# Optimization experiments

Hardware: AMD Instinct MI355X
Metric: run time of the kernel (lower is better)

Reference implementation:

```python
import jax, jax.numpy as jnp
import numpy as np
import math

N_HEAD = 32
HEAD_DIM = 64
ROTARY_DIM = 32
ROTARY_BASE = 10000.0
NEG_INF = -10000.0


def _rope_cos_sin(seqlen):
    # RotaryEmbedding._update_cos_sin_cache: inv_freq over even indices of rotary_dim
    inv_freq = 1.0 / (ROTARY_BASE ** (jnp.arange(0, ROTARY_DIM, 2, dtype=jnp.float32) / ROTARY_DIM))
    t = jnp.arange(seqlen, dtype=jnp.float32)
    freqs = jnp.outer(t, inv_freq)  # [s, rd/2]
    return jnp.cos(freqs), jnp.sin(freqs)


def _apply_rotary(t, cos, sin):
    # t: [b, s, h, d]; GPT-NeoX half-rotation on first ROTARY_DIM dims, pass-through rest
    half = ROTARY_DIM // 2
    x1 = t[..., :half]
    x2 = t[..., half:ROTARY_DIM]
    x_pass = t[..., ROTARY_DIM:]
    c = cos[:, None, :]  # [s, 1, rd/2] -> broadcasts over (b, s, h, rd/2)
    s_ = sin[:, None, :]
    return jnp.concatenate([x1 * c - x2 * s_, x1 * s_ + x2 * c, x_pass], axis=-1)


def setup_inputs() -> dict:
    key = jax.random.key(0)
    k1, k2, k3, k4, k5 = jax.random.split(key, 5)
    b, s, e = 2, 2048, 2048
    return {
        "x": jax.random.normal(k1, (b, s, e), dtype=jnp.float32),
        "Wqkv": jax.random.normal(k2, (e, 3 * e), dtype=jnp.float32) * 0.02,
        "bqkv": jax.random.normal(k3, (3 * e,), dtype=jnp.float32) * 0.02,
        "Wout": jax.random.normal(k4, (e, e), dtype=jnp.float32) * 0.02,
        "bout": jax.random.normal(k5, (e,), dtype=jnp.float32) * 0.02,
    }


def reference(x, Wqkv, bqkv, Wout, bout):
    b, s, e = x.shape
    # QKV projection -> [b, s, 3, h, d]
    qkv = (x @ Wqkv + bqkv).reshape(b, s, 3, N_HEAD, HEAD_DIM)
    cos, sin = _rope_cos_sin(s)
    q = _apply_rotary(qkv[:, :, 0], cos, sin)
    k = _apply_rotary(qkv[:, :, 1], cos, sin)
    v = qkv[:, :, 2]
    # Attention (SelfAttention/CrossAttention math, fp32, materialized scores)
    scale = 1.0 / math.sqrt(HEAD_DIM)
    scores = jnp.einsum('bthd,bshd->bhts', q, k * scale)  # [b, h, s, s]
    rows = jnp.arange(s)[:, None]
    cols = jnp.arange(s)[None, :]
    causal_mask = cols > rows  # seqlen_q == seqlen_k
    scores = jnp.where(causal_mask, NEG_INF, scores)
    attn = jax.nn.softmax(scores, axis=-1)
    out = jnp.einsum('bhts,bshd->bthd', attn, v).reshape(b, s, e)
    return out @ Wout + bout
```

## Files before the change

### kernel.cpp

```cpp
#include <hip/hip_runtime.h>


typedef _Float16 half8 __attribute__((ext_vector_type(8)));
typedef _Float16 half4 __attribute__((ext_vector_type(4)));
typedef float floatx4 __attribute__((ext_vector_type(4)));

#define GLD_LDS16(gp, sp)                                        \
  __builtin_amdgcn_global_load_lds(                              \
      (__attribute__((address_space(1))) void*)(gp),             \
      (__attribute__((address_space(3))) void*)(sp), 16, 0, 0)

__device__ __forceinline__ floatx4 mfma16(half8 a, half8 b, floatx4 c) {
  return __builtin_amdgcn_mfma_f32_16x16x32_f16(a, b, c, 0, 0, 0);
}
__device__ __forceinline__ floatx4 mfma16k16(half4 a, half4 b, floatx4 c) {
  return __builtin_amdgcn_mfma_f32_16x16x16f16(a, b, c, 0, 0, 0);
}

__global__ __launch_bounds__(256) void cvt_x_kernel(const float* __restrict__ x,
                                                    _Float16* __restrict__ xh) {
  int idx = blockIdx.x * 256 + threadIdx.x;
  const floatx4* p = (const floatx4*)x + (size_t)idx * 2;
  floatx4 a = p[0], b = p[1];
  half8 o;
#pragma unroll
  for (int j = 0; j < 4; ++j) { o[j] = (_Float16)a[j]; o[4 + j] = (_Float16)b[j]; }
  *((half8*)xh + idx) = o;
}

__global__ __launch_bounds__(256) void cvt_wt_kernel(const float* __restrict__ W,
                                                     _Float16* __restrict__ Wt,
                                                     int Kd, int Nd) {
  __shared__ float tile[64][65];
  int n0 = blockIdx.x * 64, k0 = blockIdx.y * 64;
  int tid = threadIdx.x;
#pragma unroll
  for (int it = 0; it < 4; ++it) {
    int r = (tid >> 4) + it * 16;
    int c = (tid & 15) * 4;
    floatx4 v = *(const floatx4*)(W + (size_t)(k0 + r) * Nd + n0 + c);
    tile[r][c + 0] = v[0]; tile[r][c + 1] = v[1];
    tile[r][c + 2] = v[2]; tile[r][c + 3] = v[3];
  }
  __syncthreads();
#pragma unroll
  for (int it = 0; it < 2; ++it) {
    int r = (tid >> 3) + it * 32;
    int c = (tid & 7) * 8;
    half8 o;
#pragma unroll
    for (int j = 0; j < 8; ++j) o[j] = (_Float16)tile[c + j][r];
    *(half8*)(Wt + (size_t)(n0 + r) * Kd + k0 + c) = o;
  }
}

template <int MODE>
__global__ __launch_bounds__(256) void gemm_f16_kernel(
    const _Float16* __restrict__ A, const _Float16* __restrict__ Bt,
    const float* __restrict__ bias, int Kd, int Nd,
    _Float16* __restrict__ Qd, _Float16* __restrict__ Kkd,
    _Float16* __restrict__ Vd, float* __restrict__ Co) {
  __shared__ __align__(16) _Float16 sA[128 * 64];
  __shared__ __align__(16) _Float16 sB[128 * 64];
  int tid = threadIdx.x, w = tid >> 6, l = tid & 63;
  int lr = l & 15, lq = l >> 4;
  int m0 = blockIdx.y * 128, n0 = blockIdx.x * 128;
  int wrow = (w >> 1) * 64, wcol = (w & 1) * 64;

  floatx4 z4 = {0.f, 0.f, 0.f, 0.f};
  floatx4 acc[4][4];
#pragma unroll
  for (int i = 0; i < 4; ++i)
#pragma unroll
    for (int j = 0; j < 4; ++j) acc[i][j] = z4;

  int srow = l >> 3;
  int slot = (l & 7) ^ srow;
  const _Float16* aG = A + (size_t)(m0 + w * 32 + srow) * Kd + slot * 8;
  const _Float16* bG = Bt + (size_t)(n0 + w * 32 + srow) * Kd + slot * 8;
  _Float16* sAw = &sA[w * 2048];
  _Float16* sBw = &sB[w * 2048];

  for (int kt = 0; kt < Kd; kt += 64) {
#pragma unroll
    for (int t = 0; t < 4; ++t) {
      GLD_LDS16(aG + (size_t)t * 8 * Kd + kt, sAw + t * 512);
      GLD_LDS16(bG + (size_t)t * 8 * Kd + kt, sBw + t * 512);
    }
    __syncthreads();
#pragma unroll
    for (int ks = 0; ks < 2; ++ks) {
      half8 af[4], bf[4];
#pragma unroll
      for (int i = 0; i < 4; ++i) {
        int ar = wrow + i * 16 + lr;
        int br = wcol + i * 16 + lr;
        int sl = (((ks << 2) | lq) ^ (lr & 7)) * 8;
        af[i] = *(const half8*)&sA[ar * 64 + sl];
        bf[i] = *(const half8*)&sB[br * 64 + sl];
      }
#pragma unroll
      for (int i = 0; i < 4; ++i)
#pragma unroll
        for (int j = 0; j < 4; ++j) acc[i][j] = mfma16(af[i], bf[j], acc[i][j]);
    }
    __syncthreads();
  }

  if (MODE == 0) {
    int which = n0 >> 11;
    _Float16* dst = (which == 0) ? Qd : (which == 1) ? Kkd : Vd;
#pragma unroll
    for (int j = 0; j < 4; ++j) {
      int n = n0 + wcol + j * 16 + lr;
      float bj = bias[n];
      int hh = (n & 2047) >> 6, dd = n & 63;
#pragma unroll
      for (int i = 0; i < 4; ++i)
#pragma unroll
        for (int r = 0; r < 4; ++r) {
          int m = m0 + wrow + i * 16 + lq * 4 + r;
          int bb = m >> 11, t = m & 2047;
          dst[((size_t)(bb * 32 + hh) * 2048 + (size_t)t) * 64 + dd] =
              (_Float16)(acc[i][j][r] + bj);
        }
    }
  } else {
#pragma unroll
    for (int j = 0; j < 4; ++j) {
      int n = n0 + wcol + j * 16 + lr;
      float bj = bias[n];
#pragma unroll
      for (int i = 0; i < 4; ++i)
#pragma unroll
        for (int r = 0; r < 4; ++r) {
          int m = m0 + wrow + i * 16 + lq * 4 + r;
          Co[(size_t)m * Nd + n] = acc[i][j][r] + bj;
        }
    }
  }
}

__global__ __launch_bounds__(256) void rope_kernel(_Float16* __restrict__ Qp,
                                                   _Float16* __restrict__ Kp) {
  int idx = blockIdx.x * 256 + threadIdx.x;
  int t = idx & 2047;
  int bh = (idx >> 11) & 63;
  _Float16* base = ((idx >> 17) ? Kp : Qp) + ((size_t)bh * 2048 + t) * 64;
  half8* hp = (half8*)base;
  half8 h0 = hp[0], h1 = hp[1], h2 = hp[2], h3 = hp[3];
  float v[32];
#pragma unroll
  for (int j = 0; j < 8; ++j) {
    v[j] = (float)h0[j];      v[8 + j] = (float)h1[j];
    v[16 + j] = (float)h2[j]; v[24 + j] = (float)h3[j];
  }
  float o[32];
#pragma unroll
  for (int j = 0; j < 16; ++j) {
    float freq = __expf(-(float)j * 0.57564627324851148f);
    float ang = (float)t * freq;
    float cs = cosf(ang), sn = sinf(ang);
    o[j] = v[j] * cs - v[j + 16] * sn;
    o[j + 16] = v[j] * sn + v[j + 16] * cs;
  }
  half8 g0, g1, g2, g3;
#pragma unroll
  for (int j = 0; j < 8; ++j) {
    g0[j] = (_Float16)o[j];      g1[j] = (_Float16)o[8 + j];
    g2[j] = (_Float16)o[16 + j]; g3[j] = (_Float16)o[24 + j];
  }
  hp[0] = g0; hp[1] = g1; hp[2] = g2; hp[3] = g3;
}

__global__ __launch_bounds__(256) void vtrans_kernel(const _Float16* __restrict__ V,
                                                     _Float16* __restrict__ Vt) {
  __shared__ __align__(16) _Float16 tile[64][72];
  int s0 = blockIdx.x * 64;
  int bh = blockIdx.y;
  const _Float16* Vb = V + (size_t)bh * 2048 * 64;
  _Float16* Vtb = Vt + (size_t)bh * 64 * 2048;
  int tid = threadIdx.x;
#pragma unroll
  for (int it = 0; it < 2; ++it) {
    int r = (tid >> 3) + it * 32;
    int cc = (tid & 7) * 8;
    *(half8*)&tile[r][cc] = *(const half8*)(Vb + (size_t)(s0 + r) * 64 + cc);
  }
  __syncthreads();
#pragma unroll
  for (int it = 0; it < 2; ++it) {
    int r = (tid >> 3) + it * 32;
    int cc = (tid & 7) * 8;
    half8 o;
#pragma unroll
    for (int j = 0; j < 8; ++j) o[j] = tile[cc + j][r];
    *(half8*)(Vtb + (size_t)r * 2048 + s0 + cc) = o;
  }
}

__global__ __launch_bounds__(256, 3) void attn_kernel(
    const _Float16* __restrict__ Q, const _Float16* __restrict__ Kk,
    const _Float16* __restrict__ Vt, _Float16* __restrict__ O) {
  constexpr int S = 2048;
  int bh = blockIdx.x;
  int qt = 15 - (int)blockIdx.y;
  int bb = bh >> 5, hh = bh & 31;
  const _Float16* Qb = Q + (size_t)bh * S * 64;
  const _Float16* Kb = Kk + (size_t)bh * S * 64;
  const _Float16* Vb = Vt + (size_t)bh * 64 * S;

  __shared__ __align__(16) _Float16 sK[128 * 72];
  __shared__ __align__(16) _Float16 sVt[64 * 136];

  int tid = threadIdx.x, w = tid >> 6, l = tid & 63;
  int lr = l & 15, quad = l >> 4;
  int q0 = qt * 128;

  half8 qf[2][2];
#pragma unroll
  for (int qtl = 0; qtl < 2; ++qtl)
#pragma unroll
    for (int ks = 0; ks < 2; ++ks) {
      half8 v = *(const half8*)(Qb + (size_t)(q0 + w * 32 + qtl * 16 + lr) * 64 +
                                ks * 32 + quad * 8);
      qf[qtl][ks] = v * (_Float16)0.18033688f;
    }

  floatx4 z4 = {0.f, 0.f, 0.f, 0.f};
  floatx4 Oa[4][2];
  float m_i[2] = {-1e30f, -1e30f}, l_i[2] = {0.f, 0.f};
#pragma unroll
  for (int dt = 0; dt < 4; ++dt)
#pragma unroll
    for (int qtl = 0; qtl < 2; ++qtl) Oa[dt][qtl] = z4;

  int rk = tid >> 3, ck = (tid & 7) * 8;
  int rv = tid >> 4, cv = (tid & 15) * 8;
  const _Float16* Kst = Kb + (size_t)rk * 64 + ck;
  const _Float16* Vst = Vb + (size_t)rv * S + cv;
  half8 kpre[4], vpre[4];
#pragma unroll
  for (int it = 0; it < 4; ++it) {
    kpre[it] = *(const half8*)(Kst + (size_t)it * 32 * 64);
    vpre[it] = *(const half8*)(Vst + (size_t)it * 16 * S);
  }

  for (int jt = 0; jt <= qt; ++jt) {
#pragma unroll
    for (int it = 0; it < 4; ++it) {
      *(half8*)&sK[(rk + it * 32) * 72 + ck] = kpre[it];
      *(half8*)&sVt[(rv + it * 16) * 136 + cv] = vpre[it];
    }
    if (jt < qt) {
      int kv1 = (jt + 1) * 128;
#pragma unroll
      for (int it = 0; it < 4; ++it) {
        kpre[it] = *(const half8*)(Kst + (size_t)(kv1 + it * 32) * 64);
        vpre[it] = *(const half8*)(Vst + kv1 + (size_t)it * 16 * S);
      }
    }
    __syncthreads();

    floatx4 Sa[2][8];
#pragma unroll
    for (int qtl = 0; qtl < 2; ++qtl)
#pragma unroll
      for (int kvt = 0; kvt < 8; ++kvt) Sa[qtl][kvt] = z4;
#pragma unroll
    for (int ks = 0; ks < 2; ++ks) {
#pragma unroll
      for (int kvt = 0; kvt < 8; ++kvt) {
        half8 kf = *(const half8*)&sK[(kvt * 16 + lr) * 72 + ks * 32 + quad * 8];
        Sa[0][kvt] = mfma16(kf, qf[0][ks], Sa[0][kvt]);
        Sa[1][kvt] = mfma16(kf, qf[1][ks], Sa[1][kvt]);
      }
    }

    if (jt == qt) {
#pragma unroll
      for (int qtl = 0; qtl < 2; ++qtl) {
        int q_loc = w * 32 + qtl * 16 + lr;
#pragma unroll
        for (int kvt = 0; kvt < 8; ++kvt) {
          int kv_base = kvt * 16 + quad * 4;
#pragma unroll
          for (int r = 0; r < 4; ++r)
            if (kv_base + r > q_loc) Sa[qtl][kvt][r] = -1e30f;
        }
      }
    }

#pragma unroll
    for (int qtl = 0; qtl < 2; ++qtl) {
      float mx = Sa[qtl][0][0];
#pragma unroll
      for (int kvt = 0; kvt < 8; ++kvt)
#pragma unroll
        for (int r = 0; r < 4; ++r) mx = fmaxf(mx, Sa[qtl][kvt][r]);
      mx = fmaxf(mx, __shfl_xor(mx, 16));
      mx = fmaxf(mx, __shfl_xor(mx, 32));
      float mnew = fmaxf(m_i[qtl], mx);
      float alpha = __builtin_amdgcn_exp2f(m_i[qtl] - mnew);
      m_i[qtl] = mnew;
      float rs = 0.f;
#pragma unroll
      for (int kvt = 0; kvt < 8; ++kvt)
#pragma unroll
        for (int r = 0; r < 4; ++r) {
          float p = __builtin_amdgcn_exp2f(Sa[qtl][kvt][r] - mnew);
          Sa[qtl][kvt][r] = p;
          rs += p;
        }
      rs += __shfl_xor(rs, 16);
      rs += __shfl_xor(rs, 32);
      l_i[qtl] = l_i[qtl] * alpha + rs;
#pragma unroll
      for (int dt = 0; dt < 4; ++dt) Oa[dt][qtl] *= alpha;
    }

#pragma unroll
    for (int kvt = 0; kvt < 8; ++kvt) {
      half4 vf[4];
#pragma unroll
      for (int dt = 0; dt < 4; ++dt)
        vf[dt] = *(const half4*)&sVt[(dt * 16 + lr) * 136 + kvt * 16 + quad * 4];
      half4 pf[2];
#pragma unroll
      for (int qtl = 0; qtl < 2; ++qtl) {
        pf[qtl][0] = (_Float16)Sa[qtl][kvt][0];
        pf[qtl][1] = (_Float16)Sa[qtl][kvt][1];
        pf[qtl][2] = (_Float16)Sa[qtl][kvt][2];
        pf[qtl][3] = (_Float16)Sa[qtl][kvt][3];
      }
#pragma unroll
      for (int dt = 0; dt < 4; ++dt)
#pragma unroll
        for (int qtl = 0; qtl < 2; ++qtl)
          Oa[dt][qtl] = mfma16k16(vf[dt], pf[qtl], Oa[dt][qtl]);
    }
    __syncthreads();
  }

  float inv0 = 1.0f / l_i[0], inv1 = 1.0f / l_i[1];
#pragma unroll
  for (int dt = 0; dt < 4; ++dt)
#pragma unroll
    for (int qtl = 0; qtl < 2; ++qtl) {
      float inv = qtl ? inv1 : inv0;
      floatx4 o = Oa[dt][qtl];
      half4 h;
      h[0] = (_Float16)(o[0] * inv); h[1] = (_Float16)(o[1] * inv);
      h[2] = (_Float16)(o[2] * inv); h[3] = (_Float16)(o[3] * inv);
      *(half4*)&sK[(w * 32 + qtl * 16 + lr) * 72 + dt * 16 + quad * 4] = h;
    }
  __syncthreads();
#pragma unroll
  for (int it = 0; it < 2; ++it) {
    int row = (tid >> 2) + it * 64;
    int t = q0 + row;
    _Float16* orow = O + ((size_t)(bb * 2048 + t)) * 2048 + hh * 64;
#pragma unroll
    for (int cc = 0; cc < 2; ++cc) {
      int col = (tid & 3) * 16 + cc * 8;
      *(half8*)(orow + col) = *(const half8*)&sK[row * 72 + col];
    }
  }
}

extern "C" void kernel_launch(void* const* d_in, const int* in_sizes, int n_in,
                              void* d_out, int out_size, void* d_ws, size_t ws_size,
                              hipStream_t stream) {
  (void)in_sizes; (void)n_in; (void)out_size; (void)ws_size;
  const float* x = (const float*)d_in[0];
  const float* Wqkv = (const float*)d_in[1];
  const float* bqkv = (const float*)d_in[2];
  const float* Wout = (const float*)d_in[3];
  const float* bout = (const float*)d_in[4];
  float* out = (float*)d_out;
  char* ws = (char*)d_ws;

  _Float16* xh    = (_Float16*)(ws + 0);
  _Float16* Vth   = (_Float16*)(ws + 0);
  _Float16* wqkvt = (_Float16*)(ws + 16777216);
  _Float16* Oh    = (_Float16*)(ws + 16777216);
  _Float16* Qh    = (_Float16*)(ws + 41943040);
  _Float16* Kh    = (_Float16*)(ws + 58720256);
  _Float16* Vh    = (_Float16*)(ws + 75497472);
  _Float16* woutt = (_Float16*)(ws + 92274688);

  cvt_x_kernel<<<4096, 256, 0, stream>>>(x, xh);
  cvt_wt_kernel<<<dim3(96, 32), 256, 0, stream>>>(Wqkv, wqkvt, 2048, 6144);
  cvt_wt_kernel<<<dim3(32, 32), 256, 0, stream>>>(Wout, woutt, 2048, 2048);
  gemm_f16_kernel<0><<<dim3(48, 32), 256, 0, stream>>>(
      xh, wqkvt, bqkv, 2048, 6144, Qh, Kh, Vh, nullptr);
  rope_kernel<<<1024, 256, 0, stream>>>(Qh, Kh);
  vtrans_kernel<<<dim3(32, 64), 256, 0, stream>>>(Vh, Vth);
  attn_kernel<<<dim3(64, 16), 256, 0, stream>>>(Qh, Kh, Vth, Oh);
  gemm_f16_kernel<1><<<dim3(16, 32), 256, 0, stream>>>(
      Oh, woutt, bout, 2048, 2048, nullptr, nullptr, nullptr, out);
}
```

Baseline: 445.7 us.

## Fuse RoPE and V transpose into QKV GEMM epilogue

Applies the rotary embedding to Q and K directly in the QKV GEMM epilogue using per-lane sincos, and writes V transposed as half4 vectors straight from the accumulators. This removes the separate rope and vtrans kernels along with their extra global memory round trips and launches. The epilogue now relies on each warp's 64-column slice covering exactly one head, and it computes sincos per element. Q and K stores remain scalar, strided fp16 writes.

```diff
diff --git a/kernel.cpp b/kernel.cpp
--- a/kernel.cpp
+++ b/kernel.cpp
@@ -109,27 +109,49 @@
 
   if (MODE == 0) {
     int which = n0 >> 11;
-    _Float16* dst = (which == 0) ? Qd : (which == 1) ? Kkd : Vd;
+    float bj[4];
+#pragma unroll
+    for (int j = 0; j < 4; ++j) bj[j] = bias[n0 + wcol + j * 16 + lr];
+    int hh = ((n0 & 2047) + wcol) >> 6;
+    if (which == 2) {
+#pragma unroll
+      for (int j = 0; j < 4; ++j) {
+        int dd = j * 16 + lr;
+#pragma unroll
+        for (int i = 0; i < 4; ++i) {
+          int m = m0 + wrow + i * 16 + lq * 4;
+          int bb = m >> 11, t = m & 2047;
+          half4 h;
+#pragma unroll
+          for (int r = 0; r < 4; ++r) h[r] = (_Float16)(acc[i][j][r] + bj[j]);
+          *(half4*)&Vd[(((size_t)(bb * 32 + hh)) * 64 + dd) * 2048 + t] = h;
+        }
+      }
+    } else {
+      _Float16* dst = which ? Kkd : Qd;
+      float freq = __expf(-(float)lr * 0.57564627324851148f);
+#pragma unroll
+      for (int i = 0; i < 4; ++i)
+#pragma unroll
+        for (int r = 0; r < 4; ++r) {
+          int m = m0 + wrow + i * 16 + lq * 4 + r;
+          int bb = m >> 11, t = m & 2047;
+          float sn, cs;
+          sincosf((float)t * freq, &sn, &cs);
+          float x1 = acc[i][0][r] + bj[0];
+          float x2 = acc[i][1][r] + bj[1];
+          _Float16* row = dst + ((size_t)(bb * 32 + hh) * 2048 + (size_t)t) * 64;
+          row[lr]      = (_Float16)(x1 * cs - x2 * sn);
+          row[lr + 16] = (_Float16)(x1 * sn + x2 * cs);
+          row[lr + 32] = (_Float16)(acc[i][2][r] + bj[2]);
+          row[lr + 48] = (_Float16)(acc[i][3][r] + bj[3]);
+        }
+    }
+  } else {
 #pragma unroll
     for (int j = 0; j < 4; ++j) {
       int n = n0 + wcol + j * 16 + lr;
       float bj = bias[n];
-      int hh = (n & 2047) >> 6, dd = n & 63;
-#pragma unroll
-      for (int i = 0; i < 4; ++i)
-#pragma unroll
-        for (int r = 0; r < 4; ++r) {
-          int m = m0 + wrow + i * 16 + lq * 4 + r;
-          int bb = m >> 11, t = m & 2047;
-          dst[((size_t)(bb * 32 + hh) * 2048 + (size_t)t) * 64 + dd] =
-              (_Float16)(acc[i][j][r] + bj);
-        }
-    }
-  } else {
-#pragma unroll
-    for (int j = 0; j < 4; ++j) {
-      int n = n0 + wcol + j * 16 + lr;
-      float bj = bias[n];
 #pragma unroll
       for (int i = 0; i < 4; ++i)
 #pragma unroll
@@ -138,64 +160,6 @@
           Co[(size_t)m * Nd + n] = acc[i][j][r] + bj;
         }
     }
-  }
-}
-
-__global__ __launch_bounds__(256) void rope_kernel(_Float16* __restrict__ Qp,
-                                                   _Float16* __restrict__ Kp) {
-  int idx = blockIdx.x * 256 + threadIdx.x;
-  int t = idx & 2047;
-  int bh = (idx >> 11) & 63;
-  _Float16* base = ((idx >> 17) ? Kp : Qp) + ((size_t)bh * 2048 + t) * 64;
-  half8* hp = (half8*)base;
-  half8 h0 = hp[0], h1 = hp[1], h2 = hp[2], h3 = hp[3];
-  float v[32];
-#pragma unroll
-  for (int j = 0; j < 8; ++j) {
-    v[j] = (float)h0[j];      v[8 + j] = (float)h1[j];
-    v[16 + j] = (float)h2[j]; v[24 + j] = (float)h3[j];
-  }
-  float o[32];
-#pragma unroll
-  for (int j = 0; j < 16; ++j) {
-    float freq = __expf(-(float)j * 0.57564627324851148f);
-    float ang = (float)t * freq;
-    float cs = cosf(ang), sn = sinf(ang);
-    o[j] = v[j] * cs - v[j + 16] * sn;
-    o[j + 16] = v[j] * sn + v[j + 16] * cs;
-  }
-  half8 g0, g1, g2, g3;
-#pragma unroll
-  for (int j = 0; j < 8; ++j) {
-    g0[j] = (_Float16)o[j];      g1[j] = (_Float16)o[8 + j];
-    g2[j] = (_Float16)o[16 + j]; g3[j] = (_Float16)o[24 + j];
-  }
-  hp[0] = g0; hp[1] = g1; hp[2] = g2; hp[3] = g3;
-}
-
-__global__ __launch_bounds__(256) void vtrans_kernel(const _Float16* __restrict__ V,
-                                                     _Float16* __restrict__ Vt) {
-  __shared__ __align__(16) _Float16 tile[64][72];
-  int s0 = blockIdx.x * 64;
-  int bh = blockIdx.y;
-  const _Float16* Vb = V + (size_t)bh * 2048 * 64;
-  _Float16* Vtb = Vt + (size_t)bh * 64 * 2048;
-  int tid = threadIdx.x;
-#pragma unroll
-  for (int it = 0; it < 2; ++it) {
-    int r = (tid >> 3) + it * 32;
-    int cc = (tid & 7) * 8;
-    *(half8*)&tile[r][cc] = *(const half8*)(Vb + (size_t)(s0 + r) * 64 + cc);
-  }
-  __syncthreads();
-#pragma unroll
-  for (int it = 0; it < 2; ++it) {
-    int r = (tid >> 3) + it * 32;
-    int cc = (tid & 7) * 8;
-    half8 o;
-#pragma unroll
-    for (int j = 0; j < 8; ++j) o[j] = tile[cc + j][r];
-    *(half8*)(Vtb + (size_t)r * 2048 + s0 + cc) = o;
   }
 }
 
@@ -381,21 +345,18 @@
   char* ws = (char*)d_ws;
 
   _Float16* xh    = (_Float16*)(ws + 0);
-  _Float16* Vth   = (_Float16*)(ws + 0);
   _Float16* wqkvt = (_Float16*)(ws + 16777216);
   _Float16* Oh    = (_Float16*)(ws + 16777216);
   _Float16* Qh    = (_Float16*)(ws + 41943040);
   _Float16* Kh    = (_Float16*)(ws + 58720256);
-  _Float16* Vh    = (_Float16*)(ws + 75497472);
+  _Float16* Vth   = (_Float16*)(ws + 75497472);
   _Float16* woutt = (_Float16*)(ws + 92274688);
 
   cvt_x_kernel<<<4096, 256, 0, stream>>>(x, xh);
   cvt_wt_kernel<<<dim3(96, 32), 256, 0, stream>>>(Wqkv, wqkvt, 2048, 6144);
   cvt_wt_kernel<<<dim3(32, 32), 256, 0, stream>>>(Wout, woutt, 2048, 2048);
   gemm_f16_kernel<0><<<dim3(48, 32), 256, 0, stream>>>(
-      xh, wqkvt, bqkv, 2048, 6144, Qh, Kh, Vh, nullptr);
-  rope_kernel<<<1024, 256, 0, stream>>>(Qh, Kh);
-  vtrans_kernel<<<dim3(32, 64), 256, 0, stream>>>(Vh, Vth);
+      xh, wqkvt, bqkv, 2048, 6144, Qh, Kh, Vth, nullptr);
   attn_kernel<<<dim3(64, 16), 256, 0, stream>>>(Qh, Kh, Vth, Oh);
   gemm_f16_kernel<1><<<dim3(16, 32), 256, 0, stream>>>(
       Oh, woutt, bout, 2048, 2048, nullptr, nullptr, nullptr, out);
```

Result: faster. 432.9 us (-2.9%).
